# Optimization experiments

Measured on AMD Instinct MI355X. Metric: run time of the kernel, lower is better.

Reference implementation:

```python
import jax, jax.numpy as jnp
import numpy as np

B, K, D, H = 4, 2048, 768, 12
HD = D // H
NEG = -1e30  # stands in for -inf in the additive mask


def setup_inputs() -> dict:
    key = jax.random.key(0)
    ks = jax.random.split(key, 11)
    s = 1.0 / np.sqrt(D)
    inp = {
        "x": jax.random.normal(ks[0], (B, K, D), jnp.float32),
        "is_context": jax.random.randint(ks[1], (B, K), 0, 2) > 0,
        "Wq": jax.random.normal(ks[2], (D, D), jnp.float32) * s,
        "bq": jax.random.normal(ks[3], (D,), jnp.float32) * 0.01,
        "Wk": jax.random.normal(ks[4], (D, D), jnp.float32) * s,
        "bk": jax.random.normal(ks[5], (D,), jnp.float32) * 0.01,
        "Wv": jax.random.normal(ks[6], (D, D), jnp.float32) * s,
        "bv": jax.random.normal(ks[7], (D,), jnp.float32) * 0.01,
        "Wo": jax.random.normal(ks[8], (D, D), jnp.float32) * s,
        "bo": jax.random.normal(ks[9], (D,), jnp.float32) * 0.01,
    }
    return inp


def reference(x, is_context, Wq, bq, Wk, bk, Wv, bv, Wo, bo):
    b, k_len, d = x.shape
    scale = 1.0 / jnp.sqrt(jnp.asarray(HD, x.dtype))
    # torch nn.Linear: y = x @ W.T + b
    q = (x @ Wq.T + bq).reshape(b, k_len, H, HD).transpose(0, 2, 1, 3)  # [B,H,K,hd]
    kk = (x @ Wk.T + bk).reshape(b, k_len, H, HD).transpose(0, 2, 1, 3)
    v = (x @ Wv.T + bv).reshape(b, k_len, H, HD).transpose(0, 2, 1, 3)

    ctx = is_context  # [B,K] bool
    # allowed[b,i,j]: context rows attend only to context cols; target rows attend to all
    allowed = (ctx[:, :, None] & ctx[:, None, :]) | (~ctx)[:, :, None]  # [B,K,K]

    scores = jnp.einsum("bhqd,bhkd->bhqk", q, kk) * scale  # [B,H,K,K]
    scores = jnp.where(allowed[:, None, :, :], scores, NEG)
    attn = jax.nn.softmax(scores, axis=-1)
    out = jnp.einsum("bhqk,bhkd->bhqd", attn, v)  # [B,H,K,hd]
    out = out.transpose(0, 2, 1, 3).reshape(b, k_len, d)
    return out @ Wo.T + bo
```

## Files before the change

kernel.cpp:

```cpp
#include <hip/hip_runtime.h>
#include <hip/hip_bf16.h>

constexpr int BATCH = 4;
constexpr int SEQ   = 2048;
constexpr int DIM   = 768;
constexpr int NH    = 12;
constexpr int HDIM  = 64;

typedef __attribute__((ext_vector_type(8))) short bf16x8;
typedef __attribute__((ext_vector_type(4))) float f32x4;
typedef __attribute__((ext_vector_type(4))) short s16x4;

__device__ inline short f2bf(float f) {
    union { float f; unsigned u; } v; v.f = f;
    unsigned r = (v.u + 0x7fff + ((v.u >> 16) & 1)) >> 16;
    return (short)r;
}

__device__ inline unsigned pack_bf16x2(float a, float b) {
    union { __hip_bfloat162 h; unsigned u; } c;
    c.h = __float22bfloat162_rn(make_float2(a, b));
    return c.u;
}

__device__ inline float fast_exp2(float x) {
#if __has_builtin(__builtin_amdgcn_exp2f)
    return __builtin_amdgcn_exp2f(x);
#else
    return __expf(x * 0.6931471805599453f);
#endif
}

__device__ inline void gld16(const short* g, short* l) {
    __builtin_amdgcn_global_load_lds(
        (const __attribute__((address_space(1))) void*)g,
        (__attribute__((address_space(3))) void*)l, 16, 0, 0);
}

__device__ inline bool ctx_at(const void* p, bool isU8, int idx) {
    return isU8 ? (((const unsigned char*)p)[idx] != 0)
                : (((const int*)p)[idx] != 0);
}

__global__ __launch_bounds__(256) void prep_kernel(
    const float* __restrict__ x,  const float* __restrict__ Wq,
    const float* __restrict__ Wk, const float* __restrict__ Wv,
    const float* __restrict__ Wo,
    short* __restrict__ xb,  short* __restrict__ Wqb,
    short* __restrict__ Wkb, short* __restrict__ Wvb,
    short* __restrict__ Wob,
    const unsigned char* __restrict__ ctxm, int ctxbytes, int* __restrict__ flag) {
    const int blk = blockIdx.x;
    constexpr int XBLK = (BATCH * SEQ * DIM / 4) / 256;
    constexpr int WBLK = (DIM * DIM / 4) / 256;

    if (blk == XBLK + 4 * WBLK) {
        __shared__ int cnt;
        if (threadIdx.x == 0) cnt = 0;
        __syncthreads();
        int local = 0;
        for (int i = threadIdx.x; i < ctxbytes; i += 256)
            if ((i & 3) != 0 && ctxm[i] != 0) local++;
        atomicAdd(&cnt, local);
        __syncthreads();
        if (threadIdx.x == 0) *flag = (cnt > 0) ? 1 : 0;
        return;
    }

    const float* src; short* dst; int i;
    if (blk < XBLK) {
        src = x; dst = xb;
        i = blk * 256 + threadIdx.x;
    } else {
        const int r = blk - XBLK;
        const int w = r / WBLK;
        src = (w == 0) ? Wq : (w == 1) ? Wk : (w == 2) ? Wv : Wo;
        dst = (w == 0) ? Wqb : (w == 1) ? Wkb : (w == 2) ? Wvb : Wob;
        i = (r - w * WBLK) * 256 + threadIdx.x;
    }
    float4 v = ((const float4*)src)[i];
    s16x4 o;
    o.x = f2bf(v.x); o.y = f2bf(v.y); o.z = f2bf(v.z); o.w = f2bf(v.w);
    ((s16x4*)dst)[i] = o;
}

template <bool BF16OUT, int NSPLIT>
__global__ __launch_bounds__(256) void gemm_mfma(
    const short* __restrict__ A,
    const short* __restrict__ W0, const float* __restrict__ bias0, void* __restrict__ C0,
    const short* __restrict__ W1, const float* __restrict__ bias1, void* __restrict__ C1,
    const short* __restrict__ W2, const float* __restrict__ bias2, void* __restrict__ C2,
    float scale0) {
    constexpr int N  = DIM;
    constexpr int Kd = DIM;
    constexpr int MT = (BATCH * SEQ) / 128;
    constexpr int NTL = DIM / 128;
    constexpr int TOT = MT * NTL * NSPLIT;
    constexpr int CHUNK = TOT / 8;

    const int bid = blockIdx.x;
    const int L = (bid & 7) * CHUNK + (bid >> 3);
    const int m_idx = L / (NTL * NSPLIT);
    const int rr    = L % (NTL * NSPLIT);
    const int n_idx = rr % NTL;
    const int z     = rr / NTL;

    const short* W; const float* bias; void* C; float scale;
    if (z == 0)      { W = W0; bias = bias0; C = C0; scale = scale0; }
    else if (z == 1) { W = W1; bias = bias1; C = C1; scale = 1.f; }
    else             { W = W2; bias = bias2; C = C2; scale = 1.f; }

    const int tid  = threadIdx.x;
    const int wave = tid >> 6;
    const int lane = tid & 63;
    const int quad = lane >> 4;
    const int l16  = lane & 15;
    const int wm   = wave & 1;
    const int wn   = wave >> 1;
    const int m0   = m_idx * 128;
    const int n0   = n_idx * 128;

    __shared__ short As[128 * 32];
    __shared__ short Bs[128 * 32];

    const int srow = tid >> 2;
    const int skq  = tid & 3;
    const short* Ag = A + (size_t)(m0 + srow) * Kd + skq * 8;
    const short* Wg = W + (size_t)(n0 + srow) * Kd + skq * 8;
    short* AsP = As + srow * 32 + skq * 8;
    short* BsP = Bs + srow * 32 + skq * 8;

    f32x4 acc[4][4] = {};

    for (int kt = 0; kt < Kd; kt += 32) {
        __syncthreads();
        gld16(Ag + kt,                AsP);
        gld16(Ag + kt + 64 * Kd,      AsP + 64 * 32);
        gld16(Wg + kt,                BsP);
        gld16(Wg + kt + 64 * Kd,      BsP + 64 * 32);
        __syncthreads();

        bf16x8 af[4], bfr[4];
#pragma unroll
        for (int mt = 0; mt < 4; ++mt)
            af[mt] = *(const bf16x8*)&As[(wm * 64 + mt * 16 + l16) * 32 + quad * 8];
#pragma unroll
        for (int nt = 0; nt < 4; ++nt)
            bfr[nt] = *(const bf16x8*)&Bs[(wn * 64 + nt * 16 + l16) * 32 + quad * 8];
#pragma unroll
        for (int mt = 0; mt < 4; ++mt)
#pragma unroll
            for (int nt = 0; nt < 4; ++nt)
                acc[mt][nt] = __builtin_amdgcn_mfma_f32_16x16x32_bf16(
                    af[mt], bfr[nt], acc[mt][nt], 0, 0, 0);
    }

    float bv[4];
#pragma unroll
    for (int nt = 0; nt < 4; ++nt) bv[nt] = bias[n0 + wn * 64 + nt * 16 + l16];

#pragma unroll
    for (int mt = 0; mt < 4; ++mt)
#pragma unroll
        for (int nt = 0; nt < 4; ++nt)
#pragma unroll
            for (int reg = 0; reg < 4; ++reg) {
                const int m = m0 + wm * 64 + mt * 16 + quad * 4 + reg;
                const int n = n0 + wn * 64 + nt * 16 + l16;
                const float v = (acc[mt][nt][reg] + bv[nt]) * scale;
                if (BF16OUT) ((short*)C)[(size_t)m * N + n] = f2bf(v);
                else         ((float*)C)[(size_t)m * N + n] = v;
            }
}

__global__ __launch_bounds__(256) void vtrans_kernel(
    const short* __restrict__ Vb, short* __restrict__ Vtg) {
    const int b  = blockIdx.z;
    const int h  = blockIdx.y;
    const int k0 = blockIdx.x * 64;
    const int kl = threadIdx.x & 15;
    const int d0 = (threadIdx.x >> 4) * 4;

    s16x4 vr[4];
#pragma unroll
    for (int g = 0; g < 4; ++g)
        vr[g] = *(const s16x4*)(Vb + (size_t)(b * SEQ + k0 + g * 16 + kl) * DIM
                                + h * HDIM + d0);
#pragma unroll
    for (int i = 0; i < 4; ++i) {
        s16x4 w = {vr[0][i], vr[1][i], vr[2][i], vr[3][i]};
        *(s16x4*)(Vtg + (size_t)((b * NH + h) * HDIM + d0 + i) * SEQ + k0 + 4 * kl) = w;
    }
}

__global__ __launch_bounds__(256, 3) void attn_mfma6(
    const short* __restrict__ Qb, const short* __restrict__ Kb,
    const short* __restrict__ Vtg, const void* __restrict__ ctxp,
    const int* __restrict__ flagp, short* __restrict__ Ob) {
    const int b    = blockIdx.z;
    const int h    = blockIdx.y;
    const int q0   = blockIdx.x * 128;
    const int tid  = threadIdx.x;
    const int wave = tid >> 6;
    const int lane = tid & 63;
    const int quad = lane >> 4;
    const int l16  = lane & 15;
    const bool isU8 = (*flagp != 0);

    __shared__ short Ks[2][64 * 64];
    __shared__ short Vs[2][64 * 64];
    __shared__ short Ps[4][32 * 64];

    short* Pw = Ps[wave];

    const short* Kg = Kb + (size_t)b * SEQ * DIM + h * HDIM;
    const short* Vg = Vtg + (size_t)(b * NH + h) * HDIM * SEQ;

    const int r0 = tid >> 3;
    const int j0 = (tid & 7) ^ (r0 & 7);
    const int sw = l16 & 7;

    bf16x8 qf[2][2];
#pragma unroll
    for (int rg = 0; rg < 2; ++rg) {
        const short* qp = Qb + (size_t)(b * SEQ + q0 + wave * 32 + rg * 16 + l16) * DIM
                        + h * HDIM + quad * 8;
        qf[rg][0] = *(const bf16x8*)qp;
        qf[rg][1] = *(const bf16x8*)(qp + 32);
    }

    unsigned nmb[2][4];
#pragma unroll
    for (int rg = 0; rg < 2; ++rg)
#pragma unroll
        for (int reg = 0; reg < 4; ++reg)
            nmb[rg][reg] = ctx_at(ctxp, isU8,
                b * SEQ + q0 + wave * 32 + rg * 16 + quad * 4 + reg) ? 0u : 0xFFFFFFFFu;

    bf16x8 ones;
#pragma unroll
    for (int i = 0; i < 8; ++i) ones[i] = (short)0x3F80;

    f32x4 accl[2] = {};
    f32x4 acc[2][4] = {};

    {
        gld16(Kg + (size_t)r0 * DIM + j0 * 8,        &Ks[0][tid * 8]);
        gld16(Kg + (size_t)(r0 + 32) * DIM + j0 * 8, &Ks[0][(tid + 256) * 8]);
        gld16(Vg + (size_t)r0 * SEQ + j0 * 8,        &Vs[0][tid * 8]);
        gld16(Vg + (size_t)(r0 + 32) * SEQ + j0 * 8, &Vs[0][(tid + 256) * 8]);
    }

    constexpr int NT = SEQ / 64;
    for (int t = 0; t < NT; ++t) {
        const int k0  = t * 64;
        const int cur = t & 1;

        __syncthreads();

        if (t + 1 < NT) {
            const int kn  = k0 + 64;
            const int nxt = cur ^ 1;
            gld16(Kg + (size_t)(kn + r0) * DIM + j0 * 8,        &Ks[nxt][tid * 8]);
            gld16(Kg + (size_t)(kn + r0 + 32) * DIM + j0 * 8,   &Ks[nxt][(tid + 256) * 8]);
            gld16(Vg + (size_t)r0 * SEQ + kn + j0 * 8,          &Vs[nxt][tid * 8]);
            gld16(Vg + (size_t)(r0 + 32) * SEQ + kn + j0 * 8,   &Vs[nxt][(tid + 256) * 8]);
        }

        const short* BK = Ks[cur];
        const short* BV = Vs[cur];

        const unsigned long long kmask =
            __ballot(ctx_at(ctxp, isU8, b * SEQ + k0 + lane));
        unsigned km2[2];
#pragma unroll
        for (int gp = 0; gp < 2; ++gp) {
            const unsigned lo = (unsigned)((kmask >> (gp * 32 + l16)) & 1ull);
            const unsigned hi = (unsigned)((kmask >> (gp * 32 + 16 + l16)) & 1ull);
            km2[gp] = (lo ? 0x0000FFFFu : 0u) | (hi ? 0xFFFF0000u : 0u);
        }

        f32x4 s4[2][4] = {};
#pragma unroll
        for (int ks = 0; ks < 2; ++ks) {
            bf16x8 kf[4];
#pragma unroll
            for (int g = 0; g < 4; ++g)
                kf[g] = *(const bf16x8*)
                    &BK[(g * 16 + l16) * 64 + (((ks * 4 + quad) ^ sw)) * 8];
#pragma unroll
            for (int g = 0; g < 4; ++g) {
                s4[0][g] = __builtin_amdgcn_mfma_f32_16x16x32_bf16(qf[0][ks], kf[g], s4[0][g], 0, 0, 0);
                s4[1][g] = __builtin_amdgcn_mfma_f32_16x16x32_bf16(qf[1][ks], kf[g], s4[1][g], 0, 0, 0);
            }
        }

#pragma unroll
        for (int rg = 0; rg < 2; ++rg)
#pragma unroll
            for (int reg = 0; reg < 4; ++reg) {
                const float p0 = fast_exp2(s4[rg][0][reg]);
                const float p1 = fast_exp2(s4[rg][1][reg]);
                const float p2 = fast_exp2(s4[rg][2][reg]);
                const float p3 = fast_exp2(s4[rg][3][reg]);
                uint2 w;
                w.x = pack_bf16x2(p0, p1) & (nmb[rg][reg] | km2[0]);
                w.y = pack_bf16x2(p2, p3) & (nmb[rg][reg] | km2[1]);
                const int row = rg * 16 + quad * 4 + reg;
                const int pos = (l16 >> 1) ^ (row & 7);
                *(uint2*)&Pw[row * 64 + pos * 8 + (l16 & 1) * 4] = w;
            }

#pragma unroll
        for (int ks = 0; ks < 2; ++ks) {
            const int rpos = (ks * 4 + quad) ^ sw;
            bf16x8 pf0 = *(const bf16x8*)&Pw[l16 * 64 + rpos * 8];
            bf16x8 pf1 = *(const bf16x8*)&Pw[(16 + l16) * 64 + rpos * 8];
            accl[0] = __builtin_amdgcn_mfma_f32_16x16x32_bf16(pf0, ones, accl[0], 0, 0, 0);
            accl[1] = __builtin_amdgcn_mfma_f32_16x16x32_bf16(pf1, ones, accl[1], 0, 0, 0);
#pragma unroll
            for (int dt = 0; dt < 4; ++dt) {
                bf16x8 vf = *(const bf16x8*)
                    &BV[(dt * 16 + l16) * 64 + (((ks * 4 + quad) ^ sw)) * 8];
                acc[0][dt] = __builtin_amdgcn_mfma_f32_16x16x32_bf16(pf0, vf, acc[0][dt], 0, 0, 0);
                acc[1][dt] = __builtin_amdgcn_mfma_f32_16x16x32_bf16(pf1, vf, acc[1][dt], 0, 0, 0);
            }
        }
    }

    float inv[2][4];
#pragma unroll
    for (int rg = 0; rg < 2; ++rg)
#pragma unroll
        for (int reg = 0; reg < 4; ++reg)
            inv[rg][reg] = 1.f / accl[rg][reg];

#pragma unroll
    for (int rg = 0; rg < 2; ++rg)
#pragma unroll
        for (int dt = 0; dt < 4; ++dt)
#pragma unroll
            for (int reg = 0; reg < 4; ++reg) {
                const int q = q0 + wave * 32 + rg * 16 + quad * 4 + reg;
                Ob[(size_t)(b * SEQ + q) * DIM + h * HDIM + dt * 16 + l16] =
                    f2bf(acc[rg][dt][reg] * inv[rg][reg]);
            }
}

extern "C" void kernel_launch(void* const* d_in, const int* in_sizes, int n_in,
                              void* d_out, int out_size, void* d_ws, size_t ws_size,
                              hipStream_t stream) {
    const float* x   = (const float*)d_in[0];
    const void*  ctx = d_in[1];
    const float* Wq  = (const float*)d_in[2];
    const float* bq  = (const float*)d_in[3];
    const float* Wk  = (const float*)d_in[4];
    const float* bk  = (const float*)d_in[5];
    const float* Wv  = (const float*)d_in[6];
    const float* bv  = (const float*)d_in[7];
    const float* Wo  = (const float*)d_in[8];
    const float* bo  = (const float*)d_in[9];
    float* out = (float*)d_out;

    char* ws = (char*)d_ws;
    int* flag = (int*)ws;
    const size_t bufbf = (size_t)BATCH * SEQ * DIM * sizeof(short);
    const size_t wbuf  = (size_t)DIM * DIM * sizeof(short);
    short* xb  = (short*)(ws + 256);
    short* Qb  = (short*)(ws + 256 + bufbf);
    short* Kb  = (short*)(ws + 256 + 2 * bufbf);
    short* Vb  = (short*)(ws + 256 + 3 * bufbf);
    short* Ab  = (short*)(ws + 256 + 4 * bufbf);
    short* Vtg = (short*)(ws + 256 + 5 * bufbf);
    short* Wqb = (short*)(ws + 256 + 6 * bufbf);
    short* Wkb = (short*)(ws + 256 + 6 * bufbf + wbuf);
    short* Wvb = (short*)(ws + 256 + 6 * bufbf + 2 * wbuf);
    short* Wob = (short*)(ws + 256 + 6 * bufbf + 3 * wbuf);

    constexpr int XBLK = (BATCH * SEQ * DIM / 4) / 256;
    constexpr int WBLK = (DIM * DIM / 4) / 256;
    prep_kernel<<<XBLK + 4 * WBLK + 1, 256, 0, stream>>>(
        x, Wq, Wk, Wv, Wo, xb, Wqb, Wkb, Wvb, Wob,
        (const unsigned char*)ctx, BATCH * SEQ, flag);

    gemm_mfma<true, 3><<<dim3((DIM / 128) * ((BATCH * SEQ) / 128) * 3, 1, 1),
                          256, 0, stream>>>(
        xb, Wqb, bq, Qb, Wkb, bk, Kb, Wvb, bv, Vb, 0.125f * 1.4426950408889634f);

    dim3 gVt(SEQ / 64, NH, BATCH);
    vtrans_kernel<<<gVt, 256, 0, stream>>>(Vb, Vtg);

    dim3 gAttn(SEQ / 128, NH, BATCH);
    attn_mfma6<<<gAttn, 256, 0, stream>>>(Qb, Kb, Vtg, ctx, flag, Ab);

    gemm_mfma<false, 1><<<dim3((DIM / 128) * ((BATCH * SEQ) / 128), 1, 1),
                           256, 0, stream>>>(
        Ab, Wob, bo, out, Wob, bo, out, Wob, bo, out, 1.f);
}
```

Measured before the change: 244.0 us.

## Fuse V transpose into QKV GEMM epilogue and swizzle attention grid

The QKV projection GEMM now writes the V output directly in the head-major transposed layout the attention kernel consumes. This removes the separate transpose kernel along with its extra global read and write of V. Attention moves to a 1D grid with a swizzled block-to-(batch, head, q-chunk) mapping, meant to spread heads across chiplets/XCDs and improve K/V cache locality. The transposed stores are 8-byte chunks strided by SEQ, so write coalescing in the epilogue may get worse.

After: 246.1 us. No clear change (+0.9%).

```diff
diff --git a/kernel.cpp b/kernel.cpp
--- a/kernel.cpp
+++ b/kernel.cpp
@@ -84,7 +84,7 @@
     ((s16x4*)dst)[i] = o;
 }
 
-template <bool BF16OUT, int NSPLIT>
+template <bool BF16OUT, int NSPLIT, bool VT>
 __global__ __launch_bounds__(256) void gemm_mfma(
     const short* __restrict__ A,
     const short* __restrict__ W0, const float* __restrict__ bias0, void* __restrict__ C0,
@@ -159,6 +159,30 @@
 #pragma unroll
     for (int nt = 0; nt < 4; ++nt) bv[nt] = bias[n0 + wn * 64 + nt * 16 + l16];
 
+    if (VT && z == 2) {
+        const int tok0 = m0 + wm * 64;
+        const int bb   = tok0 >> 11;
+        const int tt   = (tok0 & (SEQ - 1)) >> 6;
+        short* Vt = (short*)C;
+#pragma unroll
+        for (int nt = 0; nt < 4; ++nt) {
+            const int n    = n0 + wn * 64 + nt * 16 + l16;
+            const int hh   = n >> 6;
+            const int dcol = n & 63;
+            short* base = Vt + ((size_t)((bb * NH + hh) * HDIM + dcol)) * SEQ
+                        + tt * 64 + 16 * quad;
+#pragma unroll
+            for (int reg = 0; reg < 4; ++reg) {
+                s16x4 o;
+#pragma unroll
+                for (int mt = 0; mt < 4; ++mt)
+                    o[mt] = f2bf(acc[mt][nt][reg] + bv[nt]);
+                *(s16x4*)(base + 4 * reg) = o;
+            }
+        }
+        return;
+    }
+
 #pragma unroll
     for (int mt = 0; mt < 4; ++mt)
 #pragma unroll
@@ -173,33 +197,15 @@
             }
 }
 
-__global__ __launch_bounds__(256) void vtrans_kernel(
-    const short* __restrict__ Vb, short* __restrict__ Vtg) {
-    const int b  = blockIdx.z;
-    const int h  = blockIdx.y;
-    const int k0 = blockIdx.x * 64;
-    const int kl = threadIdx.x & 15;
-    const int d0 = (threadIdx.x >> 4) * 4;
-
-    s16x4 vr[4];
-#pragma unroll
-    for (int g = 0; g < 4; ++g)
-        vr[g] = *(const s16x4*)(Vb + (size_t)(b * SEQ + k0 + g * 16 + kl) * DIM
-                                + h * HDIM + d0);
-#pragma unroll
-    for (int i = 0; i < 4; ++i) {
-        s16x4 w = {vr[0][i], vr[1][i], vr[2][i], vr[3][i]};
-        *(s16x4*)(Vtg + (size_t)((b * NH + h) * HDIM + d0 + i) * SEQ + k0 + 4 * kl) = w;
-    }
-}
-
-__global__ __launch_bounds__(256, 3) void attn_mfma6(
+__global__ __launch_bounds__(256, 3) void attn_mfma6x(
     const short* __restrict__ Qb, const short* __restrict__ Kb,
     const short* __restrict__ Vtg, const void* __restrict__ ctxp,
     const int* __restrict__ flagp, short* __restrict__ Ob) {
-    const int b    = blockIdx.z;
-    const int h    = blockIdx.y;
-    const int q0   = blockIdx.x * 128;
+    const int swz  = (blockIdx.x & 7) * 96 + (blockIdx.x >> 3);
+    const int qc   = swz & 15;
+    const int h    = (swz >> 4) % NH;
+    const int b    = swz / (16 * NH);
+    const int q0   = qc * 128;
     const int tid  = threadIdx.x;
     const int wave = tid >> 6;
     const int lane = tid & 63;
@@ -369,7 +375,6 @@
     short* xb  = (short*)(ws + 256);
     short* Qb  = (short*)(ws + 256 + bufbf);
     short* Kb  = (short*)(ws + 256 + 2 * bufbf);
-    short* Vb  = (short*)(ws + 256 + 3 * bufbf);
     short* Ab  = (short*)(ws + 256 + 4 * bufbf);
     short* Vtg = (short*)(ws + 256 + 5 * bufbf);
     short* Wqb = (short*)(ws + 256 + 6 * bufbf);
@@ -383,17 +388,14 @@
         x, Wq, Wk, Wv, Wo, xb, Wqb, Wkb, Wvb, Wob,
         (const unsigned char*)ctx, BATCH * SEQ, flag);
 
-    gemm_mfma<true, 3><<<dim3((DIM / 128) * ((BATCH * SEQ) / 128) * 3, 1, 1),
-                          256, 0, stream>>>(
-        xb, Wqb, bq, Qb, Wkb, bk, Kb, Wvb, bv, Vb, 0.125f * 1.4426950408889634f);
-
-    dim3 gVt(SEQ / 64, NH, BATCH);
-    vtrans_kernel<<<gVt, 256, 0, stream>>>(Vb, Vtg);
-
-    dim3 gAttn(SEQ / 128, NH, BATCH);
-    attn_mfma6<<<gAttn, 256, 0, stream>>>(Qb, Kb, Vtg, ctx, flag, Ab);
-
-    gemm_mfma<false, 1><<<dim3((DIM / 128) * ((BATCH * SEQ) / 128), 1, 1),
-                           256, 0, stream>>>(
+    gemm_mfma<true, 3, true><<<dim3((DIM / 128) * ((BATCH * SEQ) / 128) * 3, 1, 1),
+                                256, 0, stream>>>(
+        xb, Wqb, bq, Qb, Wkb, bk, Kb, Wvb, bv, Vtg, 0.125f * 1.4426950408889634f);
+
+    attn_mfma6x<<<dim3(SEQ / 128 * NH * BATCH, 1, 1), 256, 0, stream>>>(
+        Qb, Kb, Vtg, ctx, flag, Ab);
+
+    gemm_mfma<false, 1, false><<<dim3((DIM / 128) * ((BATCH * SEQ) / 128), 1, 1),
+                                  256, 0, stream>>>(
         Ab, Wob, bo, out, Wob, bo, out, Wob, bo, out, 1.f);
 }
```
